# Performance work log

Hardware: AMD Instinct MI355X
Metric: run time of the kernel (lower is better)

## Reference

```python
import jax, jax.numpy as jnp
import numpy as np

N_EMBD = 1024
N_HEAD = 16
HEAD_SIZE = N_EMBD // N_HEAD


def setup_inputs() -> dict:
    key = jax.random.key(0)
    k1, k2, k3, k4 = jax.random.split(key, 4)
    x = jax.random.normal(k1, (2, 2048, N_EMBD), dtype=jnp.float32)
    # nn.Linear weights: stored as [out, in]; apply as x @ W.T
    scale = 1.0 / np.sqrt(N_EMBD)
    W_kqv = jax.random.uniform(k2, (3 * N_EMBD, N_EMBD), jnp.float32, -scale, scale)
    W_proj = jax.random.uniform(k3, (N_EMBD, N_EMBD), jnp.float32, -scale, scale)
    b_proj = jax.random.uniform(k4, (N_EMBD,), jnp.float32, -scale, scale)
    return {"x": x, "W_kqv": W_kqv, "W_proj": W_proj, "b_proj": b_proj}


def reference(x, W_kqv, W_proj, b_proj):
    B, T, C = x.shape
    H, D = N_HEAD, HEAD_SIZE
    kqv = x @ W_kqv.T  # [B, T, 3C]
    # source splits as k, q, v (k first)
    k, q, v = jnp.split(kqv, 3, axis=-1)
    k = k.reshape(B, T, H, D).transpose(0, 2, 1, 3)  # [B,H,T,D]
    q = q.reshape(B, T, H, D).transpose(0, 2, 1, 3)
    v = v.reshape(B, T, H, D).transpose(0, 2, 1, 3)
    wei = jnp.einsum('bhqd,bhkd->bhqk', q, k) * (D ** -0.5)  # [B,H,T,T]
    causal = jnp.tril(jnp.ones((T, T), dtype=bool))
    wei = jnp.where(causal[None, None], wei, -jnp.inf)
    wei = jax.nn.softmax(wei, axis=-1)
    out = jnp.einsum('bhqk,bhkd->bhqd', wei, v)  # [B,H,T,D]
    out = out.transpose(0, 2, 1, 3).reshape(B, T, C)
    return out @ W_proj.T + b_proj
```

## Files before the change

### kernel.cpp

```cpp
#include <hip/hip_runtime.h>
#include <cstdint>


typedef __bf16 bf16x8 __attribute__((ext_vector_type(8)));
typedef unsigned short u16x8 __attribute__((ext_vector_type(8)));
typedef float f32x4 __attribute__((ext_vector_type(4)));

__device__ __forceinline__ float bf2f(unsigned short u) {
    return __uint_as_float(((unsigned int)u) << 16);
}
__device__ __forceinline__ unsigned short f2bf(float f) {
    unsigned int u = __float_as_uint(f);
    u += 0x7fffu + ((u >> 16) & 1u);
    return (unsigned short)(u >> 16);
}
__device__ __forceinline__ void stC(float* p, float v) { *p = v; }
__device__ __forceinline__ void stC(unsigned short* p, float v) { *p = f2bf(v); }

__device__ __forceinline__ void gl2lds16(const unsigned short* g, unsigned short* l) {
    __builtin_amdgcn_global_load_lds(
        (__attribute__((address_space(1))) void*)g,
        (__attribute__((address_space(3))) void*)l, 16, 0, 0);
}

__device__ __forceinline__ unsigned short* swz(unsigned short* base, int row, int col) {
    const int off = ((row << 7) + (col << 1)) ^ ((row & 7) << 4);
    return (unsigned short*)((char*)base + off);
}
__device__ __forceinline__ const unsigned short* swz(const unsigned short* base, int row, int col) {
    const int off = ((row << 7) + (col << 1)) ^ ((row & 7) << 4);
    return (const unsigned short*)((const char*)base + off);
}

__device__ __forceinline__ void cvt8(const float* __restrict__ s, unsigned short* __restrict__ d) {
    const f32x4 a = *(const f32x4*)s;
    const f32x4 b = *(const f32x4*)(s + 4);
    u16x8 o;
    o[0] = f2bf(a[0]); o[1] = f2bf(a[1]); o[2] = f2bf(a[2]); o[3] = f2bf(a[3]);
    o[4] = f2bf(b[0]); o[5] = f2bf(b[1]); o[6] = f2bf(b[2]); o[7] = f2bf(b[3]);
    *(u16x8*)d = o;
}
__global__ __launch_bounds__(256) void cvt_bf16_3(
    const float* __restrict__ s0, unsigned short* __restrict__ d0, int n0,
    const float* __restrict__ s1, unsigned short* __restrict__ d1, int n1,
    const float* __restrict__ s2, unsigned short* __restrict__ d2, int n2)
{
    const int t = blockIdx.x * 256 + threadIdx.x;
    const int S = gridDim.x * 256;
    for (int i = t; i < n0 / 8; i += S) cvt8(s0 + (size_t)i * 8, d0 + (size_t)i * 8);
    for (int i = t; i < n1 / 8; i += S) cvt8(s1 + (size_t)i * 8, d1 + (size_t)i * 8);
    for (int i = t; i < n2 / 8; i += S) cvt8(s2 + (size_t)i * 8, d2 + (size_t)i * 8);
}

template <typename TOut>
__device__ __forceinline__ void gemm_body(
    const unsigned short* __restrict__ A,
    const unsigned short* __restrict__ B,
    const float* __restrict__ bias,
    TOut* __restrict__ C,
    int M, int N, int K)
{
    __shared__ __align__(16) unsigned short As[128 * 32];
    __shared__ __align__(16) unsigned short Bs[128 * 32];

    const int tid = threadIdx.x;
    const int bn = blockIdx.x, bm = blockIdx.y;
    const int w = tid >> 6, lane = tid & 63;
    const int quad = lane >> 4, l16 = lane & 15;
    const int wm = (w >> 1) * 64, wn = (w & 1) * 64;

    f32x4 acc[4][4] = {};

    const int srow = w * 16 + (lane >> 2);
    const int scol = (lane & 3) * 8;
    const unsigned short* Ag = &A[(size_t)(bm * 128 + srow) * K + scol];
    const unsigned short* Bg = &B[(size_t)(bn * 128 + srow) * K + scol];
    unsigned short* AsW = &As[(w * 16) * 32];
    unsigned short* BsW = &Bs[(w * 16) * 32];

    for (int k0 = 0; k0 < K; k0 += 32) {
        gl2lds16(Ag + k0, AsW);
        gl2lds16(Ag + (size_t)64 * K + k0, AsW + 64 * 32);
        gl2lds16(Bg + k0, BsW);
        gl2lds16(Bg + (size_t)64 * K + k0, BsW + 64 * 32);
        __syncthreads();

        bf16x8 af[4], bfr[4];
#pragma unroll
        for (int t = 0; t < 4; t++) {
            af[t]  = *(const bf16x8*)&As[(wm + t * 16 + l16) * 32 + quad * 8];
            bfr[t] = *(const bf16x8*)&Bs[(wn + t * 16 + l16) * 32 + quad * 8];
        }
#pragma unroll
        for (int mt = 0; mt < 4; mt++)
#pragma unroll
            for (int nt = 0; nt < 4; nt++)
                acc[mt][nt] = __builtin_amdgcn_mfma_f32_16x16x32_bf16(
                    af[mt], bfr[nt], acc[mt][nt], 0, 0, 0);
        __syncthreads();
    }

#pragma unroll
    for (int mt = 0; mt < 4; mt++) {
        const int row = bm * 128 + wm + mt * 16 + quad * 4;
#pragma unroll
        for (int nt = 0; nt < 4; nt++) {
            const int col = bn * 128 + wn + nt * 16 + l16;
            const float bv = bias ? bias[col] : 0.0f;
#pragma unroll
            for (int r = 0; r < 4; r++)
                stC(&C[(size_t)(row + r) * N + col], acc[mt][nt][r] + bv);
        }
    }
}

__global__ __launch_bounds__(256, 3) void gemm_qkv(
    const unsigned short* __restrict__ A, const unsigned short* __restrict__ B,
    unsigned short* __restrict__ C, int M, int N, int K)
{
    gemm_body<unsigned short>(A, B, nullptr, C, M, N, K);
}
__global__ __launch_bounds__(256, 3) void gemm_proj(
    const unsigned short* __restrict__ A, const unsigned short* __restrict__ B,
    const float* __restrict__ bias, float* __restrict__ C, int M, int N, int K)
{
    gemm_body<float>(A, B, bias, C, M, N, K);
}

__global__ __launch_bounds__(256) void attn_fused(
    const unsigned short* __restrict__ kqv,
    unsigned short* __restrict__ out)
{
    __shared__ __align__(16) unsigned short Qs[64 * 64];
    __shared__ __align__(16) unsigned short Ks[2][64 * 64];
    __shared__ __align__(16) unsigned short Vts[2][64 * 64];
    __shared__ __align__(16) unsigned short Ps[64 * 64];

    const int bh = blockIdx.x;
    const int qt = 31 - (int)blockIdx.y;
    const int b = bh >> 4, h = bh & 15;
    const int tid = threadIdx.x;
    const int w = tid >> 6;
    const int lane = tid & 63;
    const int quad = lane >> 4, l16 = lane & 15;
    const int rowBase = b * 2048;
    const int kOff = h * 64, qOff = 1024 + h * 64, vOff = 2048 + h * 64;
    const float SEXP = 0.125f * 1.4426950408889634f;
    const float MASKV = -1.0e30f;

#pragma unroll
    for (int i = 0; i < 2; i++) {
        const int v = tid + i * 256;
        const int row = v >> 3, c8 = (v & 7) * 8;
        *(u16x8*)swz(Qs, row, c8) =
            *(const u16x8*)&kqv[(size_t)(rowBase + qt * 64 + row) * 3072 + qOff + c8];
    }

    f32x4 o[4] = {};
    float l_i[4] = {0.f, 0.f, 0.f, 0.f};

    u16x8 kr[2], vr[2];
#pragma unroll
    for (int i = 0; i < 2; i++) {
        const int v = tid + i * 256;
        kr[i] = *(const u16x8*)&kqv[(size_t)(rowBase + (v >> 3)) * 3072 + kOff + (v & 7) * 8];
        vr[i] = *(const u16x8*)&kqv[(size_t)(rowBase + lane) * 3072 + vOff + (i * 4 + w) * 8];
    }

    for (int j = 0; j <= qt; j++) {
        const int cur = j & 1;
#pragma unroll
        for (int i = 0; i < 2; i++) {
            const int v = tid + i * 256;
            *(u16x8*)swz(Ks[cur], v >> 3, (v & 7) * 8) = kr[i];
            const int d8 = i * 4 + w;
#pragma unroll
            for (int u = 0; u < 8; u++)
                *swz(Vts[cur], d8 * 8 + u, lane) = vr[i][u];
        }
        __syncthreads();

        if (j < qt) {
#pragma unroll
            for (int i = 0; i < 2; i++) {
                const int v = tid + i * 256;
                kr[i] = *(const u16x8*)&kqv[(size_t)(rowBase + (j + 1) * 64 + (v >> 3)) * 3072 + kOff + (v & 7) * 8];
                vr[i] = *(const u16x8*)&kqv[(size_t)(rowBase + (j + 1) * 64 + lane) * 3072 + vOff + (i * 4 + w) * 8];
            }
        }

        f32x4 s[4] = {};
#pragma unroll
        for (int ks = 0; ks < 2; ks++) {
            const bf16x8 aq = *(const bf16x8*)swz(Qs, w * 16 + l16, ks * 32 + quad * 8);
#pragma unroll
            for (int nt = 0; nt < 4; nt++) {
                const bf16x8 bk = *(const bf16x8*)swz(Ks[cur], nt * 16 + l16, ks * 32 + quad * 8);
                s[nt] = __builtin_amdgcn_mfma_f32_16x16x32_bf16(aq, bk, s[nt], 0, 0, 0);
            }
        }

        if (j == qt) {
            const int rowl = w * 16 + quad * 4;
#pragma unroll
            for (int nt = 0; nt < 4; nt++) {
                const int coll = nt * 16 + l16;
#pragma unroll
                for (int r = 0; r < 4; r++)
                    if (coll > rowl + r) s[nt][r] = MASKV;
            }
        }

#pragma unroll
        for (int nt = 0; nt < 4; nt++) {
#pragma unroll
            for (int r = 0; r < 4; r++) {
                const float p = exp2f(s[nt][r] * SEXP);
                l_i[r] += p;
                *swz(Ps, w * 16 + quad * 4 + r, nt * 16 + l16) = f2bf(p);
            }
        }
        __syncthreads();

#pragma unroll
        for (int ks = 0; ks < 2; ks++) {
            const bf16x8 ap = *(const bf16x8*)swz(Ps, w * 16 + l16, ks * 32 + quad * 8);
#pragma unroll
            for (int nt = 0; nt < 4; nt++) {
                const bf16x8 bv = *(const bf16x8*)swz(Vts[cur], nt * 16 + l16, ks * 32 + quad * 8);
                o[nt] = __builtin_amdgcn_mfma_f32_16x16x32_bf16(ap, bv, o[nt], 0, 0, 0);
            }
        }
    }

    float linv[4];
#pragma unroll
    for (int r = 0; r < 4; r++) {
        float t = l_i[r];
        t += __shfl_xor(t, 1);
        t += __shfl_xor(t, 2);
        t += __shfl_xor(t, 4);
        t += __shfl_xor(t, 8);
        linv[r] = 1.0f / t;
    }

#pragma unroll
    for (int nt = 0; nt < 4; nt++) {
        const int col = h * 64 + nt * 16 + l16;
#pragma unroll
        for (int r = 0; r < 4; r++)
            out[(size_t)(rowBase + qt * 64 + w * 16 + quad * 4 + r) * 1024 + col] =
                f2bf(o[nt][r] * linv[r]);
    }
}

extern "C" void kernel_launch(void* const* d_in, const int* in_sizes, int n_in,
                              void* d_out, int out_size, void* d_ws, size_t ws_size,
                              hipStream_t stream) {
    const float* x     = (const float*)d_in[0];
    const float* Wkqv  = (const float*)d_in[1];
    const float* Wproj = (const float*)d_in[2];
    const float* bproj = (const float*)d_in[3];
    float* out = (float*)d_out;

    unsigned short* kqv    = (unsigned short*)d_ws;
    unsigned short* attn   = kqv    + (size_t)4096 * 3072;
    unsigned short* xb     = attn   + (size_t)4096 * 1024;
    unsigned short* wkqvb  = xb     + (size_t)4096 * 1024;
    unsigned short* wprojb = wkqvb  + (size_t)3072 * 1024;

    cvt_bf16_3<<<dim3(512), dim3(256), 0, stream>>>(
        x, xb, 4096 * 1024, Wkqv, wkqvb, 3072 * 1024, Wproj, wprojb, 1024 * 1024);

    gemm_qkv<<<dim3(24, 32), dim3(256), 0, stream>>>(
        xb, wkqvb, kqv, 4096, 3072, 1024);

    attn_fused<<<dim3(32, 32), dim3(256), 0, stream>>>(kqv, attn);

    gemm_proj<<<dim3(8, 32), dim3(256), 0, stream>>>(
        attn, wprojb, bproj, out, 4096, 1024, 1024);
}
```

Before: 184.8 us.

## Shrink proj GEMM tile, keep Q in registers, add MFMA priority hints

The output-projection GEMM moves from 128x128 to 64x128 tiles and launches twice as many blocks (512 instead of 256). With 256 CUs, the old grid gave only one block per CU. In the attention kernel, the Q fragments are loaded straight from global memory into registers, so the Q shared-memory tile and its repeated LDS reads are gone. The MFMA sections are wrapped in s_setprio raise and lower. The trade-off is lower per-block reuse in the projection GEMM and slightly more register pressure in attention.

```diff
diff --git a/kernel.cpp b/kernel.cpp
--- a/kernel.cpp
+++ b/kernel.cpp
@@ -52,13 +52,9 @@
     for (int i = t; i < n2 / 8; i += S) cvt8(s2 + (size_t)i * 8, d2 + (size_t)i * 8);
 }
 
-template <typename TOut>
-__device__ __forceinline__ void gemm_body(
-    const unsigned short* __restrict__ A,
-    const unsigned short* __restrict__ B,
-    const float* __restrict__ bias,
-    TOut* __restrict__ C,
-    int M, int N, int K)
+__global__ __launch_bounds__(256, 3) void gemm_qkv(
+    const unsigned short* __restrict__ A, const unsigned short* __restrict__ B,
+    unsigned short* __restrict__ C, int M, int N, int K)
 {
     __shared__ __align__(16) unsigned short As[128 * 32];
     __shared__ __align__(16) unsigned short Bs[128 * 32];
@@ -106,32 +102,75 @@
 #pragma unroll
         for (int nt = 0; nt < 4; nt++) {
             const int col = bn * 128 + wn + nt * 16 + l16;
-            const float bv = bias ? bias[col] : 0.0f;
 #pragma unroll
             for (int r = 0; r < 4; r++)
-                stC(&C[(size_t)(row + r) * N + col], acc[mt][nt][r] + bv);
-        }
-    }
-}
-
-__global__ __launch_bounds__(256, 3) void gemm_qkv(
-    const unsigned short* __restrict__ A, const unsigned short* __restrict__ B,
-    unsigned short* __restrict__ C, int M, int N, int K)
-{
-    gemm_body<unsigned short>(A, B, nullptr, C, M, N, K);
-}
-__global__ __launch_bounds__(256, 3) void gemm_proj(
+                stC(&C[(size_t)(row + r) * N + col], acc[mt][nt][r]);
+        }
+    }
+}
+
+__global__ __launch_bounds__(256) void gemm_proj(
     const unsigned short* __restrict__ A, const unsigned short* __restrict__ B,
     const float* __restrict__ bias, float* __restrict__ C, int M, int N, int K)
 {
-    gemm_body<float>(A, B, bias, C, M, N, K);
+    __shared__ __align__(16) unsigned short As[64 * 32];
+    __shared__ __align__(16) unsigned short Bs[128 * 32];
+
+    const int tid = threadIdx.x;
+    const int bn = blockIdx.x, bm = blockIdx.y;
+    const int w = tid >> 6, lane = tid & 63;
+    const int quad = lane >> 4, l16 = lane & 15;
+    const int wm = (w >> 1) * 32, wn = (w & 1) * 64;
+
+    f32x4 acc[2][4] = {};
+
+    const int srow = w * 16 + (lane >> 2);
+    const int scol = (lane & 3) * 8;
+    const unsigned short* Ag = &A[(size_t)(bm * 64 + srow) * K + scol];
+    const unsigned short* Bg = &B[(size_t)(bn * 128 + srow) * K + scol];
+    unsigned short* AsW = &As[(w * 16) * 32];
+    unsigned short* BsW = &Bs[(w * 16) * 32];
+
+    for (int k0 = 0; k0 < K; k0 += 32) {
+        gl2lds16(Ag + k0, AsW);
+        gl2lds16(Bg + k0, BsW);
+        gl2lds16(Bg + (size_t)64 * K + k0, BsW + 64 * 32);
+        __syncthreads();
+
+        bf16x8 af[2], bfr[4];
+#pragma unroll
+        for (int t = 0; t < 2; t++)
+            af[t]  = *(const bf16x8*)&As[(wm + t * 16 + l16) * 32 + quad * 8];
+#pragma unroll
+        for (int t = 0; t < 4; t++)
+            bfr[t] = *(const bf16x8*)&Bs[(wn + t * 16 + l16) * 32 + quad * 8];
+#pragma unroll
+        for (int mt = 0; mt < 2; mt++)
+#pragma unroll
+            for (int nt = 0; nt < 4; nt++)
+                acc[mt][nt] = __builtin_amdgcn_mfma_f32_16x16x32_bf16(
+                    af[mt], bfr[nt], acc[mt][nt], 0, 0, 0);
+        __syncthreads();
+    }
+
+#pragma unroll
+    for (int mt = 0; mt < 2; mt++) {
+        const int row = bm * 64 + wm + mt * 16 + quad * 4;
+#pragma unroll
+        for (int nt = 0; nt < 4; nt++) {
+            const int col = bn * 128 + wn + nt * 16 + l16;
+            const float bv = bias[col];
+#pragma unroll
+            for (int r = 0; r < 4; r++)
+                C[(size_t)(row + r) * N + col] = acc[mt][nt][r] + bv;
+        }
+    }
 }
 
 __global__ __launch_bounds__(256) void attn_fused(
     const unsigned short* __restrict__ kqv,
     unsigned short* __restrict__ out)
 {
-    __shared__ __align__(16) unsigned short Qs[64 * 64];
     __shared__ __align__(16) unsigned short Ks[2][64 * 64];
     __shared__ __align__(16) unsigned short Vts[2][64 * 64];
     __shared__ __align__(16) unsigned short Ps[64 * 64];
@@ -148,12 +187,11 @@
     const float SEXP = 0.125f * 1.4426950408889634f;
     const float MASKV = -1.0e30f;
 
-#pragma unroll
-    for (int i = 0; i < 2; i++) {
-        const int v = tid + i * 256;
-        const int row = v >> 3, c8 = (v & 7) * 8;
-        *(u16x8*)swz(Qs, row, c8) =
-            *(const u16x8*)&kqv[(size_t)(rowBase + qt * 64 + row) * 3072 + qOff + c8];
+    bf16x8 aq[2];
+    {
+        const size_t qrow = (size_t)(rowBase + qt * 64 + w * 16 + l16) * 3072 + qOff;
+        aq[0] = *(const bf16x8*)&kqv[qrow + quad * 8];
+        aq[1] = *(const bf16x8*)&kqv[qrow + 32 + quad * 8];
     }
 
     f32x4 o[4] = {};
@@ -190,15 +228,16 @@
         }
 
         f32x4 s[4] = {};
+        __builtin_amdgcn_s_setprio(1);
 #pragma unroll
         for (int ks = 0; ks < 2; ks++) {
-            const bf16x8 aq = *(const bf16x8*)swz(Qs, w * 16 + l16, ks * 32 + quad * 8);
 #pragma unroll
             for (int nt = 0; nt < 4; nt++) {
                 const bf16x8 bk = *(const bf16x8*)swz(Ks[cur], nt * 16 + l16, ks * 32 + quad * 8);
-                s[nt] = __builtin_amdgcn_mfma_f32_16x16x32_bf16(aq, bk, s[nt], 0, 0, 0);
-            }
-        }
+                s[nt] = __builtin_amdgcn_mfma_f32_16x16x32_bf16(aq[ks], bk, s[nt], 0, 0, 0);
+            }
+        }
+        __builtin_amdgcn_s_setprio(0);
 
         if (j == qt) {
             const int rowl = w * 16 + quad * 4;
@@ -222,6 +261,7 @@
         }
         __syncthreads();
 
+        __builtin_amdgcn_s_setprio(1);
 #pragma unroll
         for (int ks = 0; ks < 2; ks++) {
             const bf16x8 ap = *(const bf16x8*)swz(Ps, w * 16 + l16, ks * 32 + quad * 8);
@@ -231,6 +271,7 @@
                 o[nt] = __builtin_amdgcn_mfma_f32_16x16x32_bf16(ap, bv, o[nt], 0, 0, 0);
             }
         }
+        __builtin_amdgcn_s_setprio(0);
     }
 
     float linv[4];
@@ -277,6 +318,6 @@
 
     attn_fused<<<dim3(32, 32), dim3(256), 0, stream>>>(kqv, attn);
 
-    gemm_proj<<<dim3(8, 32), dim3(256), 0, stream>>>(
+    gemm_proj<<<dim3(8, 64), dim3(256), 0, stream>>>(
         attn, wprojb, bproj, out, 4096, 1024, 1024);
 }
```

Result: no change. 187.0 us (+1.2%).
